# Kernel tuning notes

Hardware: AMD Instinct MI355X
Metric: run time of the kernel (lower is better)

## Reference

```python
import jax, jax.numpy as jnp
import numpy as np

# Reconstructed semantics of the butterfly C++ kernel:
#  - gather rows of `data` via indices_in -> x [N, B]
#  - num_input_layers of Givens-rotation butterfly layers (pairs within 16-wide
#    blocks, XOR stride 1,2,4,8 cycling per layer)
#  - fused bias + smooth-ReLU activation (curvature-smoothed) on the first
#    num_activations rows of each 16-block
#  - num_output_layers more butterfly layers
#  - scatter result back into `data` at idx_out (forward returns data, updated)

COL_BLOCK = 16
NUM_INPUT_LAYERS = 4
NUM_OUTPUT_LAYERS = 4
NUM_ACTIVATIONS = 8
CURVATURE = 0.1


def _rotate_layer(x, ang, stride):
    # x: [N, B]; ang: [N//2]
    N = x.shape[0]
    idx = np.arange(N)
    low = idx[((idx % COL_BLOCK) & stride) == 0]  # static pair indices
    hi = low + stride
    c = jnp.cos(ang)[:, None]
    s = jnp.sin(ang)[:, None]
    xl, xh = x[low], x[hi]
    return x.at[low].set(c * xl + s * xh).at[hi].set(-s * xl + c * xh)


def setup_inputs() -> dict:
    key = jax.random.key(0)
    k1, k2, k3 = jax.random.split(key, 3)
    N, B = 4096, 8192
    num_layers = NUM_INPUT_LAYERS + NUM_OUTPUT_LAYERS
    num_blocks = N // COL_BLOCK
    data = jax.random.normal(k1, (N, B), dtype=jnp.float32)
    angles = jax.random.uniform(k2, (num_layers, N // 2), dtype=jnp.float32,
                                minval=-np.pi, maxval=np.pi)
    biases = jax.random.normal(k3, (NUM_ACTIVATIONS * num_blocks,), dtype=jnp.float32)
    indices_in = jnp.arange(N, dtype=jnp.int32)
    idx_out = jnp.arange(N, dtype=jnp.int32)
    return {"data": data, "angles": angles, "biases": biases,
            "indices_in": indices_in, "idx_out": idx_out}


def reference(data, angles, biases, indices_in, idx_out):
    N = indices_in.shape[0]
    x = data[indices_in]  # [N, B] gather
    layer = 0
    for _ in range(NUM_INPUT_LAYERS):
        x = _rotate_layer(x, angles[layer], 1 << (layer % 4))
        layer += 1
    # fused bias + smooth ReLU on first NUM_ACTIVATIONS rows of each 16-block
    offs = np.arange(N) % COL_BLOCK
    act_rows = np.nonzero(offs < NUM_ACTIVATIONS)[0]  # block-major order matches biases layout
    b_full = jnp.zeros((N,), x.dtype).at[act_rows].set(biases)
    xa = x + b_full[:, None]
    act = 0.5 * (xa + jnp.sqrt(xa * xa + CURVATURE * CURVATURE))
    mask = jnp.asarray(offs < NUM_ACTIVATIONS)[:, None]
    x = jnp.where(mask, act, x)
    for _ in range(NUM_OUTPUT_LAYERS):
        x = _rotate_layer(x, angles[layer], 1 << (layer % 4))
        layer += 1
    return data.at[idx_out].set(x)  # scatter back (mimics in-place update)
```

## Files before the change

### kernel.cpp

```cpp
#include <hip/hip_runtime.h>


constexpr int COL_BLOCK = 16;
constexpr int TPB = 256;
constexpr int CPT = 4;
constexpr float CURV2 = 0.1f * 0.1f;

typedef float floatx4 __attribute__((ext_vector_type(4)));

template <int L>
__device__ __forceinline__ void rot_layer(floatx4 (&x)[16],
                                          const float (&cs)[8][8],
                                          const float (&sn)[8][8]) {
    constexpr int b = L & 3;
    constexpr int s = 1 << b;
#pragma unroll
    for (int j = 0; j < 8; ++j) {
        const int lo = ((j >> b) << (b + 1)) | (j & (s - 1));
        const int hi = lo + s;
        const float c = cs[L][j];
        const float sv = sn[L][j];
        const floatx4 xl = x[lo];
        const floatx4 xh = x[hi];
        x[lo] = c * xl + sv * xh;
        x[hi] = c * xh - sv * xl;
    }
}

__global__ __launch_bounds__(TPB) void butterfly_kernel(
    const float* __restrict__ data,
    const float* __restrict__ angles,
    const float* __restrict__ biases,
    const int* __restrict__ indices_in,
    const int* __restrict__ idx_out,
    float* __restrict__ out,
    int N, int B)
{
    const int tile = blockIdx.x;
    const int blk = blockIdx.y;
    const int tid = threadIdx.x;
    const int half = N >> 1;

    __shared__ float cs[8][8];
    __shared__ float sn[8][8];
    __shared__ float bs[8];
    __shared__ int rin[16];
    __shared__ int rout[16];

    if (tid < 64) {
        const int l = tid >> 3, j = tid & 7;
        const float a = angles[l * half + blk * 8 + j];
        cs[l][j] = cosf(a);
        sn[l][j] = sinf(a);
    } else if (tid < 72) {
        bs[tid - 64] = biases[blk * 8 + (tid - 64)];
    } else if (tid < 88) {
        rin[tid - 72] = indices_in[blk * 16 + (tid - 72)];
    } else if (tid < 104) {
        rout[tid - 88] = idx_out[blk * 16 + (tid - 88)];
    }
    __syncthreads();

    const int c0 = tile * (TPB * CPT) + tid * CPT;

    floatx4 x[16];
#pragma unroll
    for (int j = 0; j < 16; ++j) {
        const size_t off = (size_t)rin[j] * (size_t)B + (size_t)c0;
        x[j] = *reinterpret_cast<const floatx4*>(data + off);
    }

    rot_layer<0>(x, cs, sn);
    rot_layer<1>(x, cs, sn);
    rot_layer<2>(x, cs, sn);
    rot_layer<3>(x, cs, sn);

#pragma unroll
    for (int j = 0; j < 8; ++j) {
        const float b = bs[j];
        floatx4 v = x[j];
#pragma unroll
        for (int e = 0; e < 4; ++e) {
            const float a = v[e] + b;
            v[e] = 0.5f * (a + sqrtf(fmaf(a, a, CURV2)));
        }
        x[j] = v;
    }

    rot_layer<4>(x, cs, sn);
    rot_layer<5>(x, cs, sn);
    rot_layer<6>(x, cs, sn);
    rot_layer<7>(x, cs, sn);

#pragma unroll
    for (int j = 0; j < 16; ++j) {
        const size_t off = (size_t)rout[j] * (size_t)B + (size_t)c0;
        *reinterpret_cast<floatx4*>(out + off) = x[j];
    }
}

__global__ void mark_kernel(const int* __restrict__ idx_out,
                            int* __restrict__ mask, int N) {
    const int i = blockIdx.x * blockDim.x + threadIdx.x;
    if (i < N) mask[idx_out[i]] = 1;
}

__global__ __launch_bounds__(TPB) void copy_untouched(
    const float* __restrict__ data, float* __restrict__ out,
    const int* __restrict__ mask, int N, int B) {
    for (int row = blockIdx.x; row < N; row += gridDim.x) {
        if (mask[row]) continue;
        const floatx4* src = reinterpret_cast<const floatx4*>(data + (size_t)row * B);
        floatx4* dst = reinterpret_cast<floatx4*>(out + (size_t)row * B);
        for (int c = threadIdx.x; c < (B >> 2); c += blockDim.x)
            dst[c] = src[c];
    }
}

extern "C" void kernel_launch(void* const* d_in, const int* in_sizes, int n_in,
                              void* d_out, int out_size, void* d_ws, size_t ws_size,
                              hipStream_t stream) {
    const float* data       = (const float*)d_in[0];
    const float* angles     = (const float*)d_in[1];
    const float* biases     = (const float*)d_in[2];
    const int*   indices_in = (const int*)d_in[3];
    const int*   idx_out    = (const int*)d_in[4];
    float* out = (float*)d_out;

    const int N = in_sizes[3];
    const int B = in_sizes[0] / N;

    int* mask = (int*)d_ws;
    hipMemsetAsync(mask, 0, (size_t)N * sizeof(int), stream);
    mark_kernel<<<dim3((N + TPB - 1) / TPB), dim3(TPB), 0, stream>>>(idx_out, mask, N);

    dim3 grid(B / (TPB * CPT), N / COL_BLOCK);
    butterfly_kernel<<<grid, dim3(TPB), 0, stream>>>(
        data, angles, biases, indices_in, idx_out, out, N, B);

    copy_untouched<<<dim3(256), dim3(TPB), 0, stream>>>(data, out, mask, N, B);
}
```

Measured before the change: 247.8 us.

## Process two column chunks per block and overlap setup with data loads

Each butterfly block now handles two 1024-column chunks, which amortises the per-block setup (angle sin/cos, bias and index loads) over twice the work and halves the grid. The row-index loads move from shared memory into per-thread registers read straight from global memory. The global data loads are issued before the sin/cos computation and the barrier so their latency overlaps the setup. The workspace memset is replaced by a zeroing kernel on a static device mask. These changes raise register pressure and reduce the number of blocks available to hide memory latency.

```diff
diff --git a/kernel.cpp b/kernel.cpp
--- a/kernel.cpp
+++ b/kernel.cpp
@@ -4,6 +4,7 @@
 constexpr int COL_BLOCK = 16;
 constexpr int TPB = 256;
 constexpr int CPT = 4;
+constexpr int NCHUNK = 2;
 constexpr float CURV2 = 0.1f * 0.1f;
 
 typedef float floatx4 __attribute__((ext_vector_type(4)));
@@ -27,7 +28,34 @@
     }
 }
 
-__global__ __launch_bounds__(TPB) void butterfly_kernel(
+__device__ __forceinline__ void process16(floatx4 (&x)[16],
+                                          const float (&cs)[8][8],
+                                          const float (&sn)[8][8],
+                                          const float (&bs)[8]) {
+    rot_layer<0>(x, cs, sn);
+    rot_layer<1>(x, cs, sn);
+    rot_layer<2>(x, cs, sn);
+    rot_layer<3>(x, cs, sn);
+
+#pragma unroll
+    for (int j = 0; j < 8; ++j) {
+        const float b = bs[j];
+        floatx4 v = x[j];
+#pragma unroll
+        for (int e = 0; e < 4; ++e) {
+            const float a = v[e] + b;
+            v[e] = 0.5f * (a + sqrtf(fmaf(a, a, CURV2)));
+        }
+        x[j] = v;
+    }
+
+    rot_layer<4>(x, cs, sn);
+    rot_layer<5>(x, cs, sn);
+    rot_layer<6>(x, cs, sn);
+    rot_layer<7>(x, cs, sn);
+}
+
+__global__ __launch_bounds__(TPB) void butterfly_kernel2(
     const float* __restrict__ data,
     const float* __restrict__ angles,
     const float* __restrict__ biases,
@@ -44,24 +72,22 @@
     __shared__ float cs[8][8];
     __shared__ float sn[8][8];
     __shared__ float bs[8];
-    __shared__ int rin[16];
-    __shared__ int rout[16];
-
+
+    const int l = tid >> 3, jj = tid & 7;
+    float ang_v = 0.0f, bias_v = 0.0f;
     if (tid < 64) {
-        const int l = tid >> 3, j = tid & 7;
-        const float a = angles[l * half + blk * 8 + j];
-        cs[l][j] = cosf(a);
-        sn[l][j] = sinf(a);
+        ang_v = angles[l * half + blk * 8 + jj];
     } else if (tid < 72) {
-        bs[tid - 64] = biases[blk * 8 + (tid - 64)];
-    } else if (tid < 88) {
-        rin[tid - 72] = indices_in[blk * 16 + (tid - 72)];
-    } else if (tid < 104) {
-        rout[tid - 88] = idx_out[blk * 16 + (tid - 88)];
-    }
-    __syncthreads();
-
-    const int c0 = tile * (TPB * CPT) + tid * CPT;
+        bias_v = biases[blk * 8 + (tid - 64)];
+    }
+
+    int rin[16], rout[16];
+#pragma unroll
+    for (int j = 0; j < 16; ++j) rin[j] = indices_in[blk * COL_BLOCK + j];
+#pragma unroll
+    for (int j = 0; j < 16; ++j) rout[j] = idx_out[blk * COL_BLOCK + j];
+
+    const int c0 = tile * (NCHUNK * TPB * CPT) + tid * CPT;
 
     floatx4 x[16];
 #pragma unroll
@@ -70,42 +96,112 @@
         x[j] = *reinterpret_cast<const floatx4*>(data + off);
     }
 
-    rot_layer<0>(x, cs, sn);
-    rot_layer<1>(x, cs, sn);
-    rot_layer<2>(x, cs, sn);
-    rot_layer<3>(x, cs, sn);
-
-#pragma unroll
-    for (int j = 0; j < 8; ++j) {
-        const float b = bs[j];
-        floatx4 v = x[j];
-#pragma unroll
-        for (int e = 0; e < 4; ++e) {
-            const float a = v[e] + b;
-            v[e] = 0.5f * (a + sqrtf(fmaf(a, a, CURV2)));
-        }
-        x[j] = v;
-    }
-
-    rot_layer<4>(x, cs, sn);
-    rot_layer<5>(x, cs, sn);
-    rot_layer<6>(x, cs, sn);
-    rot_layer<7>(x, cs, sn);
-
+    if (tid < 64) {
+        cs[l][jj] = cosf(ang_v);
+        sn[l][jj] = sinf(ang_v);
+    } else if (tid < 72) {
+        bs[tid - 64] = bias_v;
+    }
+    __syncthreads();
+
+    process16(x, cs, sn, bs);
 #pragma unroll
     for (int j = 0; j < 16; ++j) {
         const size_t off = (size_t)rout[j] * (size_t)B + (size_t)c0;
         *reinterpret_cast<floatx4*>(out + off) = x[j];
     }
-}
-
-__global__ void mark_kernel(const int* __restrict__ idx_out,
-                            int* __restrict__ mask, int N) {
+
+    const int c1 = c0 + TPB * CPT;
+#pragma unroll
+    for (int j = 0; j < 16; ++j) {
+        const size_t off = (size_t)rin[j] * (size_t)B + (size_t)c1;
+        x[j] = *reinterpret_cast<const floatx4*>(data + off);
+    }
+    process16(x, cs, sn, bs);
+#pragma unroll
+    for (int j = 0; j < 16; ++j) {
+        const size_t off = (size_t)rout[j] * (size_t)B + (size_t)c1;
+        *reinterpret_cast<floatx4*>(out + off) = x[j];
+    }
+}
+
+__global__ __launch_bounds__(TPB) void butterfly_kernel1(
+    const float* __restrict__ data, const float* __restrict__ angles,
+    const float* __restrict__ biases, const int* __restrict__ indices_in,
+    const int* __restrict__ idx_out, float* __restrict__ out, int N, int B)
+{
+    const int tile = blockIdx.x;
+    const int blk = blockIdx.y;
+    const int tid = threadIdx.x;
+    const int half = N >> 1;
+
+    __shared__ float cs[8][8];
+    __shared__ float sn[8][8];
+    __shared__ float bs[8];
+
+    const int l = tid >> 3, jj = tid & 7;
+    float ang_v = 0.0f, bias_v = 0.0f;
+    if (tid < 64) ang_v = angles[l * half + blk * 8 + jj];
+    else if (tid < 72) bias_v = biases[blk * 8 + (tid - 64)];
+
+    int rin[16], rout[16];
+#pragma unroll
+    for (int j = 0; j < 16; ++j) rin[j] = indices_in[blk * COL_BLOCK + j];
+#pragma unroll
+    for (int j = 0; j < 16; ++j) rout[j] = idx_out[blk * COL_BLOCK + j];
+
+    const int c0 = tile * (TPB * CPT) + tid * CPT;
+
+    floatx4 x[16];
+#pragma unroll
+    for (int j = 0; j < 16; ++j) {
+        const size_t off = (size_t)rin[j] * (size_t)B + (size_t)c0;
+        x[j] = *reinterpret_cast<const floatx4*>(data + off);
+    }
+
+    if (tid < 64) { cs[l][jj] = cosf(ang_v); sn[l][jj] = sinf(ang_v); }
+    else if (tid < 72) bs[tid - 64] = bias_v;
+    __syncthreads();
+
+    process16(x, cs, sn, bs);
+#pragma unroll
+    for (int j = 0; j < 16; ++j) {
+        const size_t off = (size_t)rout[j] * (size_t)B + (size_t)c0;
+        *reinterpret_cast<floatx4*>(out + off) = x[j];
+    }
+}
+
+constexpr int MAX_MASK_N = 1 << 16;
+__device__ int g_mask[MAX_MASK_N];
+
+__global__ void zero_mask_kernel(int N) {
+    const int i = blockIdx.x * blockDim.x + threadIdx.x;
+    if (i < N) g_mask[i] = 0;
+}
+
+__global__ void mark_kernel_g(const int* __restrict__ idx_out, int N) {
+    const int i = blockIdx.x * blockDim.x + threadIdx.x;
+    if (i < N) g_mask[idx_out[i]] = 1;
+}
+
+__global__ __launch_bounds__(TPB) void copy_untouched_g(
+    const float* __restrict__ data, float* __restrict__ out, int N, int B) {
+    for (int row = blockIdx.x; row < N; row += gridDim.x) {
+        if (g_mask[row]) continue;
+        const floatx4* src = reinterpret_cast<const floatx4*>(data + (size_t)row * B);
+        floatx4* dst = reinterpret_cast<floatx4*>(out + (size_t)row * B);
+        for (int c = threadIdx.x; c < (B >> 2); c += blockDim.x)
+            dst[c] = src[c];
+    }
+}
+
+__global__ void mark_kernel_ws(const int* __restrict__ idx_out,
+                               int* __restrict__ mask, int N) {
     const int i = blockIdx.x * blockDim.x + threadIdx.x;
     if (i < N) mask[idx_out[i]] = 1;
 }
 
-__global__ __launch_bounds__(TPB) void copy_untouched(
+__global__ __launch_bounds__(TPB) void copy_untouched_ws(
     const float* __restrict__ data, float* __restrict__ out,
     const int* __restrict__ mask, int N, int B) {
     for (int row = blockIdx.x; row < N; row += gridDim.x) {
@@ -130,13 +226,33 @@
     const int N = in_sizes[3];
     const int B = in_sizes[0] / N;
 
-    int* mask = (int*)d_ws;
-    hipMemsetAsync(mask, 0, (size_t)N * sizeof(int), stream);
-    mark_kernel<<<dim3((N + TPB - 1) / TPB), dim3(TPB), 0, stream>>>(idx_out, mask, N);
-
-    dim3 grid(B / (TPB * CPT), N / COL_BLOCK);
-    butterfly_kernel<<<grid, dim3(TPB), 0, stream>>>(
-        data, angles, biases, indices_in, idx_out, out, N, B);
-
-    copy_untouched<<<dim3(256), dim3(TPB), 0, stream>>>(data, out, mask, N, B);
-}
+    const dim3 tpb(TPB);
+    const dim3 mgrid((N + TPB - 1) / TPB);
+
+    const bool use_global_mask = (N <= MAX_MASK_N);
+    if (use_global_mask) {
+        zero_mask_kernel<<<mgrid, tpb, 0, stream>>>(N);
+        mark_kernel_g<<<mgrid, tpb, 0, stream>>>(idx_out, N);
+    } else {
+        int* mask = (int*)d_ws;
+        hipMemsetAsync(mask, 0, (size_t)N * sizeof(int), stream);
+        mark_kernel_ws<<<mgrid, tpb, 0, stream>>>(idx_out, (int*)d_ws, N);
+    }
+
+    if (B % (NCHUNK * TPB * CPT) == 0) {
+        dim3 grid(B / (NCHUNK * TPB * CPT), N / COL_BLOCK);
+        butterfly_kernel2<<<grid, tpb, 0, stream>>>(
+            data, angles, biases, indices_in, idx_out, out, N, B);
+    } else {
+        dim3 grid(B / (TPB * CPT), N / COL_BLOCK);
+        butterfly_kernel1<<<grid, tpb, 0, stream>>>(
+            data, angles, biases, indices_in, idx_out, out, N, B);
+    }
+
+    if (use_global_mask) {
+        copy_untouched_g<<<dim3(256), tpb, 0, stream>>>(data, out, N, B);
+    } else {
+        copy_untouched_ws<<<dim3(256), tpb, 0, stream>>>(
+            data, out, (const int*)d_ws, N, B);
+    }
+}
```

After: 251.0 us. Within noise of the previous version (+1.3%).
